# Kernel optimization log

Hardware: AMD Instinct MI355X
Metric: run time of the kernel (lower is better)

## Reference

```python
import jax, jax.numpy as jnp
import numpy as np

WINDOW_SIZE = 11

def _gauss_window(ws):
    x = np.arange(ws, dtype=np.float32)
    g = np.exp(-0.5 * (x - (ws - 1) / 2.0) ** 2 / 0.5 ** 2)
    g = g / g.sum()
    w = np.outer(g, g)
    return jnp.asarray(w[None, None], dtype=jnp.float32)  # [1,1,ws,ws]

_SOBEL_X = jnp.asarray(np.array([[-1, 0, 1], [-2, 0, 2], [-1, 0, 1]], np.float32)[None, None])
_SOBEL_Y = jnp.asarray(np.array([[1, 2, 1], [0, 0, 0], [-1, -2, -1]], np.float32)[None, None])

def _conv2d(x, k, pad):
    # x: [B,1,H,W], k: [1,1,kh,kw], 'same'-style explicit padding
    return jax.lax.conv_general_dilated(
        x, k, window_strides=(1, 1), padding=[(pad, pad), (pad, pad)],
        dimension_numbers=("NCHW", "OIHW", "NCHW"))

def _sobel(x):
    return jnp.abs(_conv2d(x, _SOBEL_X, 1)) + jnp.abs(_conv2d(x, _SOBEL_Y, 1))

def setup_inputs() -> dict:
    key = jax.random.key(0)
    kA, kB, kF, kS = jax.random.split(key, 4)
    shape = (32, 1, 512, 512)
    return {
        "image_A": jax.random.uniform(kA, shape, dtype=jnp.float32),
        "image_B": jax.random.uniform(kB, shape, dtype=jnp.float32),
        "image_fused": jax.random.uniform(kF, shape, dtype=jnp.float32),
        "fuse_scheme": jax.random.randint(kS, (32,), 0, 2, dtype=jnp.int64),
    }

def reference(image_A, image_B, image_fused, fuse_scheme):
    ws = WINDOW_SIZE
    pad = ws // 2
    window = _gauss_window(ws)
    scheme = fuse_scheme.reshape(-1, 1, 1, 1)

    # masked construction of the pseudo-reference image_AB
    avg_AB = (image_A + image_B) * 0.5
    max_AB = jnp.maximum(image_A, image_B)
    image_AB = jnp.where(scheme == 0, avg_AB,
                         jnp.where(scheme == 1, max_AB, jnp.zeros_like(image_fused)))
    l_loss = jnp.mean(jnp.abs(image_AB - image_fused))

    # SSIM-style local statistics
    mu_A = _conv2d(image_A, window, pad)
    mu_B = _conv2d(image_B, window, pad)
    mu_f = _conv2d(image_fused, window, pad)
    sigma_A_sq = _conv2d(image_A ** 2, window, pad) - mu_A ** 2
    sigma_B_sq = _conv2d(image_B ** 2, window, pad) - mu_B ** 2
    sigma_f_sq = _conv2d(image_fused ** 2, window, pad) - mu_f ** 2
    sigma_Af = _conv2d(image_A * image_fused, window, pad) - mu_A * mu_f
    sigma_Bf = _conv2d(image_B * image_fused, window, pad) - mu_B * mu_f

    C = 0.03 ** 2
    cs1 = (2 * sigma_Af + C) / (sigma_A_sq + sigma_f_sq + C)
    cs2 = (2 * sigma_Bf + C) / (sigma_B_sq + sigma_f_sq + C)
    cs_map = 0.5 * cs1 + 0.5 * cs2
    cs_loss = 1.0 - (cs_map.mean() + 1.0) / 2.0

    grad_loss = jnp.mean(jnp.abs(_sobel(image_fused) -
                                 jnp.maximum(_sobel(image_A), _sobel(image_B))))
    return l_loss + 0.0 * cs_loss + grad_loss
```

## Files before the change

kernel.cpp:

```cpp
#include <hip/hip_runtime.h>

#define BATCH 32
#define H 512
#define W 512
#define N_TOT (BATCH * H * W)
#define BAND 8
#define NBLOCKS 1024


template <bool USE_PARTIALS>
__global__ __launch_bounds__(256)
void fusion_loss_kernel(const float* __restrict__ A,
                        const float* __restrict__ B,
                        const float* __restrict__ F,
                        const int* __restrict__ scheme_arr,
                        float* __restrict__ sink)
{
    __shared__ float red[4];

    const int t    = threadIdx.x;
    const int lane = t & 63;
    const int ty   = t >> 6;
    const int wave = blockIdx.x * 4 + ty;
    const int half = wave & 1;
    const int band = wave >> 1;
    const int b    = band >> 6;
    const int r0   = (band & 63) << 3;
    const int x0   = (half << 8) + (lane << 2);
    const int base = b * (H * W);
    const int scheme = scheme_arr[b];
    const bool has_l = (x0 > 0);
    const bool has_r = (x0 + 4 < W);

    const float* __restrict__ imgs[3] = {A, B, F};

    float4 rc[3][4];
    float  rl[3][4];
    float  rh[3][4];

    auto load_row = [&](int y, int slot) {
        const bool rv = (unsigned)y < (unsigned)H;
#pragma unroll
        for (int im = 0; im < 3; ++im) {
            float4 c = make_float4(0.f, 0.f, 0.f, 0.f);
            float lf = 0.f, rt = 0.f;
            if (rv) {
                const float* row = imgs[im] + base + y * W;
                c  = *reinterpret_cast<const float4*>(row + x0);
                lf = has_l ? row[x0 - 1] : 0.f;
                rt = has_r ? row[x0 + 4] : 0.f;
            }
            rc[im][slot] = c;
            rl[im][slot] = lf;
            rh[im][slot] = rt;
        }
    };

    load_row(r0 - 1, 3);
    load_row(r0,     0);
    load_row(r0 + 1, 1);

    float acc = 0.f;

#pragma unroll
    for (int k = 0; k < BAND; ++k) {
        if (k < BAND - 1) load_row(r0 + k + 2, (k + 2) & 3);

        const int sm = (k + 3) & 3;
        const int sc = k & 3;
        const int sp = (k + 1) & 3;

        float sobM[4];
#pragma unroll
        for (int im = 0; im < 3; ++im) {
            float gx[4], gy[4];
            {
                const float4 c4 = rc[im][sm];
                const float v[6] = {rl[im][sm], c4.x, c4.y, c4.z, c4.w, rh[im][sm]};
#pragma unroll
                for (int j = 0; j < 4; ++j) {
                    gx[j] = v[j + 2] - v[j];
                    gy[j] = v[j] + 2.f * v[j + 1] + v[j + 2];
                }
            }
            {
                const float4 c4 = rc[im][sc];
                const float v[6] = {rl[im][sc], c4.x, c4.y, c4.z, c4.w, rh[im][sc]};
#pragma unroll
                for (int j = 0; j < 4; ++j)
                    gx[j] += 2.f * (v[j + 2] - v[j]);
            }
            {
                const float4 c4 = rc[im][sp];
                const float v[6] = {rl[im][sp], c4.x, c4.y, c4.z, c4.w, rh[im][sp]};
#pragma unroll
                for (int j = 0; j < 4; ++j) {
                    gx[j] += v[j + 2] - v[j];
                    gy[j] -= v[j] + 2.f * v[j + 1] + v[j + 2];
                }
            }
#pragma unroll
            for (int j = 0; j < 4; ++j) {
                const float sob = fabsf(gx[j]) + fabsf(gy[j]);
                if (im == 0)      sobM[j] = sob;
                else if (im == 1) sobM[j] = fmaxf(sobM[j], sob);
                else              acc += fabsf(sob - sobM[j]);
            }
        }

        {
            const float4 a4 = rc[0][sc], b4 = rc[1][sc], f4 = rc[2][sc];
            const float av[4] = {a4.x, a4.y, a4.z, a4.w};
            const float bv[4] = {b4.x, b4.y, b4.z, b4.w};
            const float fv[4] = {f4.x, f4.y, f4.z, f4.w};
#pragma unroll
            for (int j = 0; j < 4; ++j) {
                const float ab = (scheme == 0) ? 0.5f * (av[j] + bv[j])
                               : (scheme == 1) ? fmaxf(av[j], bv[j])
                               : 0.f;
                acc += fabsf(ab - fv[j]);
            }
        }
    }

#pragma unroll
    for (int off = 32; off > 0; off >>= 1)
        acc += __shfl_down(acc, off, 64);
    if (lane == 0) red[ty] = acc;
    __syncthreads();
    if (t == 0) {
        const float s = red[0] + red[1] + red[2] + red[3];
        if (USE_PARTIALS)
            sink[blockIdx.x] = s;
        else
            atomicAdd(sink, s * (1.0f / (float)N_TOT));
    }
}

__global__ __launch_bounds__(256)
void fusion_finish(const float* __restrict__ partials, float* __restrict__ out)
{
    __shared__ float red[4];
    const int t    = threadIdx.x;
    const int lane = t & 63;
    const int ty   = t >> 6;

    const float4 p = reinterpret_cast<const float4*>(partials)[t];
    float v = (p.x + p.y) + (p.z + p.w);
#pragma unroll
    for (int off = 32; off > 0; off >>= 1)
        v += __shfl_down(v, off, 64);
    if (lane == 0) red[ty] = v;
    __syncthreads();
    if (t == 0)
        out[0] = (red[0] + red[1] + red[2] + red[3]) * (1.0f / (float)N_TOT);
}

extern "C" void kernel_launch(void* const* d_in, const int* in_sizes, int n_in,
                              void* d_out, int out_size, void* d_ws, size_t ws_size,
                              hipStream_t stream)
{
    const float* A = (const float*)d_in[0];
    const float* B = (const float*)d_in[1];
    const float* F = (const float*)d_in[2];
    const int* scheme = (const int*)d_in[3];
    float* out = (float*)d_out;

    if (d_ws != nullptr && ws_size >= NBLOCKS * sizeof(float)) {
        float* partials = (float*)d_ws;
        fusion_loss_kernel<true><<<dim3(NBLOCKS), dim3(256), 0, stream>>>(
            A, B, F, scheme, partials);
        fusion_finish<<<dim3(1), dim3(256), 0, stream>>>(partials, out);
    } else {
        hipMemsetAsync(out, 0, sizeof(float), stream);
        fusion_loss_kernel<false><<<dim3(NBLOCKS), dim3(256), 0, stream>>>(
            A, B, F, scheme, out);
    }
}
```

Measured before the change: 128.7 us.

## Stage rows into an LDS ring via global_load_lds and double the band height

Replaces per-wave direct global loads of the three images, including scalar halo loads, with async global-to-LDS copies into a six-slot ring buffer shared by the block. Each block now covers a 16-row band, and wave pairs split even and odd rows while reading 3x3 windows from LDS. The aim is to remove the redundant unaligned halo loads and overlap staging of the next rows with compute. The cost is a block-wide barrier every step, added LDS traffic, and half as many blocks.

```diff
diff --git a/kernel.cpp b/kernel.cpp
--- a/kernel.cpp
+++ b/kernel.cpp
@@ -1,12 +1,21 @@
 #include <hip/hip_runtime.h>
+#include <stdint.h>
 
 #define BATCH 32
 #define H 512
 #define W 512
 #define N_TOT (BATCH * H * W)
-#define BAND 8
-#define NBLOCKS 1024
+#define BAND 16
+#define STEPS (BAND / 2)
+#define NBLOCKS (BATCH * (H / BAND))
+#define RING 6
+#define ROWF 512
+#define TRIPF (3 * ROWF)
+#define LDSF (RING * TRIPF)
 
+
+#define GAS(p) ((__attribute__((address_space(1))) void*)(p))
+#define LAS(p) ((__attribute__((address_space(3))) void*)(p))
 
 template <bool USE_PARTIALS>
 __global__ __launch_bounds__(256)
@@ -16,88 +25,91 @@
                         const int* __restrict__ scheme_arr,
                         float* __restrict__ sink)
 {
+    __shared__ float sh[LDSF];
     __shared__ float red[4];
 
     const int t    = threadIdx.x;
     const int lane = t & 63;
     const int ty   = t >> 6;
-    const int wave = blockIdx.x * 4 + ty;
-    const int half = wave & 1;
-    const int band = wave >> 1;
-    const int b    = band >> 6;
-    const int r0   = (band & 63) << 3;
-    const int x0   = (half << 8) + (lane << 2);
+    const int d    = ty >> 1;
+    const int h    = ty & 1;
+    const int blk  = blockIdx.x;
+    const int b    = blk >> 5;
+    const int band = blk & 31;
+    const int r0   = band << 4;
     const int base = b * (H * W);
     const int scheme = scheme_arr[b];
-    const bool has_l = (x0 > 0);
-    const bool has_r = (x0 + 4 < W);
 
-    const float* __restrict__ imgs[3] = {A, B, F};
+    const bool edgeL = (h == 0) && (lane == 0);
+    const bool edgeR = (h == 1) && (lane == 63);
 
-    float4 rc[3][4];
-    float  rl[3][4];
-    float  rh[3][4];
-
-    auto load_row = [&](int y, int slot) {
-        const bool rv = (unsigned)y < (unsigned)H;
-#pragma unroll
-        for (int im = 0; im < 3; ++im) {
-            float4 c = make_float4(0.f, 0.f, 0.f, 0.f);
-            float lf = 0.f, rt = 0.f;
-            if (rv) {
-                const float* row = imgs[im] + base + y * W;
-                c  = *reinterpret_cast<const float4*>(row + x0);
-                lf = has_l ? row[x0 - 1] : 0.f;
-                rt = has_r ? row[x0 + 4] : 0.f;
+    auto stage = [&](int s0, int ng) {
+        for (int i = 0; ; ++i) {
+            const int g = ty + (i << 2);
+            if (g >= ng) break;
+            const int trip = g / 6;
+            const int sub  = g - 6 * trip;
+            const int img  = sub >> 1;
+            const int hh   = sub & 1;
+            const int s    = s0 + trip;
+            const int slot = s % RING;
+            const int y    = r0 - 1 + s;
+            float* ldst = &sh[slot * TRIPF + img * ROWF + (hh << 8)];
+            if ((unsigned)y < (unsigned)H) {
+                const float* ip = (img == 0) ? A : (img == 1) ? B : F;
+                const float* gsrc = ip + base + y * W + (hh << 8) + (lane << 2);
+                __builtin_amdgcn_global_load_lds(GAS(gsrc), LAS(ldst), 16, 0, 0);
+            } else {
+                *reinterpret_cast<float4*>(ldst + (lane << 2)) =
+                    make_float4(0.f, 0.f, 0.f, 0.f);
             }
-            rc[im][slot] = c;
-            rl[im][slot] = lf;
-            rh[im][slot] = rt;
         }
     };
 
-    load_row(r0 - 1, 3);
-    load_row(r0,     0);
-    load_row(r0 + 1, 1);
+    auto load_win = [&](float (*w)[6], int seqz) {
+        const int slot = seqz % RING;
+        const float* srow = &sh[slot * TRIPF];
+        const int ci = lane << 2;
+#pragma unroll
+        for (int im = 0; im < 3; ++im) {
+            const float* rowp = srow + im * ROWF + (h << 8);
+            const float4 c = *reinterpret_cast<const float4*>(rowp + ci);
+            const int li = edgeL ? ci : ci - 1;
+            const int ri = edgeR ? ci + 3 : ci + 4;
+            float l = rowp[li];
+            float r = rowp[ri];
+            if (edgeL) l = 0.f;
+            if (edgeR) r = 0.f;
+            w[im][0] = l;   w[im][1] = c.x; w[im][2] = c.y;
+            w[im][3] = c.z; w[im][4] = c.w; w[im][5] = r;
+        }
+    };
+
+    stage(0, 24);
+    __syncthreads();
+
+    float wm[3][6], wc[3][6], wp[3][6];
+    load_win(wm, d);
 
     float acc = 0.f;
 
-#pragma unroll
-    for (int k = 0; k < BAND; ++k) {
-        if (k < BAND - 1) load_row(r0 + k + 2, (k + 2) & 3);
+    for (int p = 0; p < STEPS; ++p) {
+        if (p < STEPS - 1) stage(2 * p + 4, 12);
 
-        const int sm = (k + 3) & 3;
-        const int sc = k & 3;
-        const int sp = (k + 1) & 3;
+        load_win(wc, d + 2 * p + 1);
+        load_win(wp, d + 2 * p + 2);
 
         float sobM[4];
 #pragma unroll
         for (int im = 0; im < 3; ++im) {
             float gx[4], gy[4];
-            {
-                const float4 c4 = rc[im][sm];
-                const float v[6] = {rl[im][sm], c4.x, c4.y, c4.z, c4.w, rh[im][sm]};
 #pragma unroll
-                for (int j = 0; j < 4; ++j) {
-                    gx[j] = v[j + 2] - v[j];
-                    gy[j] = v[j] + 2.f * v[j + 1] + v[j + 2];
-                }
-            }
-            {
-                const float4 c4 = rc[im][sc];
-                const float v[6] = {rl[im][sc], c4.x, c4.y, c4.z, c4.w, rh[im][sc]};
-#pragma unroll
-                for (int j = 0; j < 4; ++j)
-                    gx[j] += 2.f * (v[j + 2] - v[j]);
-            }
-            {
-                const float4 c4 = rc[im][sp];
-                const float v[6] = {rl[im][sp], c4.x, c4.y, c4.z, c4.w, rh[im][sp]};
-#pragma unroll
-                for (int j = 0; j < 4; ++j) {
-                    gx[j] += v[j + 2] - v[j];
-                    gy[j] -= v[j] + 2.f * v[j + 1] + v[j + 2];
-                }
+            for (int j = 0; j < 4; ++j) {
+                gx[j] = (wm[im][j + 2] - wm[im][j])
+                      + 2.f * (wc[im][j + 2] - wc[im][j])
+                      + (wp[im][j + 2] - wp[im][j]);
+                gy[j] = (wm[im][j] + 2.f * wm[im][j + 1] + wm[im][j + 2])
+                      - (wp[im][j] + 2.f * wp[im][j + 1] + wp[im][j + 2]);
             }
 #pragma unroll
             for (int j = 0; j < 4; ++j) {
@@ -108,19 +120,24 @@
             }
         }
 
-        {
-            const float4 a4 = rc[0][sc], b4 = rc[1][sc], f4 = rc[2][sc];
-            const float av[4] = {a4.x, a4.y, a4.z, a4.w};
-            const float bv[4] = {b4.x, b4.y, b4.z, b4.w};
-            const float fv[4] = {f4.x, f4.y, f4.z, f4.w};
 #pragma unroll
-            for (int j = 0; j < 4; ++j) {
-                const float ab = (scheme == 0) ? 0.5f * (av[j] + bv[j])
-                               : (scheme == 1) ? fmaxf(av[j], bv[j])
-                               : 0.f;
-                acc += fabsf(ab - fv[j]);
-            }
+        for (int j = 0; j < 4; ++j) {
+            const float av = wc[0][j + 1];
+            const float bv = wc[1][j + 1];
+            const float fv = wc[2][j + 1];
+            const float ab = (scheme == 0) ? 0.5f * (av + bv)
+                           : (scheme == 1) ? fmaxf(av, bv)
+                           : 0.f;
+            acc += fabsf(ab - fv);
         }
+
+#pragma unroll
+        for (int im = 0; im < 3; ++im)
+#pragma unroll
+            for (int k = 0; k < 6; ++k)
+                wm[im][k] = wp[im][k];
+
+        __syncthreads();
     }
 
 #pragma unroll
```

After: 176.6 us. 37.2% more time.

## Process one row per wave with full-row lanes and shuffle-based halos

Applied to the files above, without the earlier changes.

Replaces the 8-row rolling band per wave with one output row per wave, where each lane covers 8 contiguous pixels of the full 512-wide row. Horizontal halo values come from cross-lane shuffles instead of extra scalar global loads, and blocks are remapped with an XCD-style interleave. This gives many more blocks (4096) with less per-thread state and a higher occupancy hint. In exchange, each input row is now loaded three times (above, center, below), which raises global/L2 traffic compared with the band reuse. The finish kernel is widened to reduce 4096 partials.

```diff
diff --git a/kernel.cpp b/kernel.cpp
--- a/kernel.cpp
+++ b/kernel.cpp
@@ -4,12 +4,13 @@
 #define H 512
 #define W 512
 #define N_TOT (BATCH * H * W)
-#define BAND 8
-#define NBLOCKS 1024
+#define ROWS_TOTAL (BATCH * H)
+#define NBLOCKS (ROWS_TOTAL / 4)
+#define WS_FLOATS NBLOCKS
 
 
 template <bool USE_PARTIALS>
-__global__ __launch_bounds__(256)
+__global__ __launch_bounds__(256, 4)
 void fusion_loss_kernel(const float* __restrict__ A,
                         const float* __restrict__ B,
                         const float* __restrict__ F,
@@ -21,117 +22,104 @@
     const int t    = threadIdx.x;
     const int lane = t & 63;
     const int ty   = t >> 6;
-    const int wave = blockIdx.x * 4 + ty;
-    const int half = wave & 1;
-    const int band = wave >> 1;
-    const int b    = band >> 6;
-    const int r0   = (band & 63) << 3;
-    const int x0   = (half << 8) + (lane << 2);
-    const int base = b * (H * W);
+
+    const int bid = blockIdx.x;
+    const int lb  = (bid & 7) * (NBLOCKS / 8) + (bid >> 3);
+
+    const int gy  = (lb << 2) | ty;
+    const int b   = gy >> 9;
+    const int y   = gy & (H - 1);
+    const int x0  = lane << 3;
     const int scheme = scheme_arr[b];
-    const bool has_l = (x0 > 0);
-    const bool has_r = (x0 + 4 < W);
 
-    const float* __restrict__ imgs[3] = {A, B, F};
+    const int off = gy * W + x0;
+    const bool vm = (y > 0);
+    const bool vp = (y < H - 1);
 
-    float4 rc[3][4];
-    float  rl[3][4];
-    float  rh[3][4];
-
-    auto load_row = [&](int y, int slot) {
-        const bool rv = (unsigned)y < (unsigned)H;
+    float4 u0[3][3], u1[3][3];
+    {
+        const float* ptr[3] = {A + off, B + off, F + off};
 #pragma unroll
         for (int im = 0; im < 3; ++im) {
-            float4 c = make_float4(0.f, 0.f, 0.f, 0.f);
-            float lf = 0.f, rt = 0.f;
-            if (rv) {
-                const float* row = imgs[im] + base + y * W;
-                c  = *reinterpret_cast<const float4*>(row + x0);
-                lf = has_l ? row[x0 - 1] : 0.f;
-                rt = has_r ? row[x0 + 4] : 0.f;
+            const float* p = ptr[im];
+            u0[im][1] = *reinterpret_cast<const float4*>(p);
+            u1[im][1] = *reinterpret_cast<const float4*>(p + 4);
+            if (vm) {
+                u0[im][0] = *reinterpret_cast<const float4*>(p - W);
+                u1[im][0] = *reinterpret_cast<const float4*>(p - W + 4);
+            } else {
+                u0[im][0] = make_float4(0.f, 0.f, 0.f, 0.f);
+                u1[im][0] = make_float4(0.f, 0.f, 0.f, 0.f);
             }
-            rc[im][slot] = c;
-            rl[im][slot] = lf;
-            rh[im][slot] = rt;
+            if (vp) {
+                u0[im][2] = *reinterpret_cast<const float4*>(p + W);
+                u1[im][2] = *reinterpret_cast<const float4*>(p + W + 4);
+            } else {
+                u0[im][2] = make_float4(0.f, 0.f, 0.f, 0.f);
+                u1[im][2] = make_float4(0.f, 0.f, 0.f, 0.f);
+            }
         }
-    };
-
-    load_row(r0 - 1, 3);
-    load_row(r0,     0);
-    load_row(r0 + 1, 1);
+    }
 
     float acc = 0.f;
 
 #pragma unroll
-    for (int k = 0; k < BAND; ++k) {
-        if (k < BAND - 1) load_row(r0 + k + 2, (k + 2) & 3);
+    for (int hh = 0; hh < 2; ++hh) {
+        const float4 a4 = hh ? u1[0][1] : u0[0][1];
+        const float4 b4 = hh ? u1[1][1] : u0[1][1];
+        const float4 f4 = hh ? u1[2][1] : u0[2][1];
+        const float av[4] = {a4.x, a4.y, a4.z, a4.w};
+        const float bv[4] = {b4.x, b4.y, b4.z, b4.w};
+        const float fv[4] = {f4.x, f4.y, f4.z, f4.w};
+#pragma unroll
+        for (int j = 0; j < 4; ++j) {
+            const float ab = (scheme == 0) ? 0.5f * (av[j] + bv[j])
+                           : (scheme == 1) ? fmaxf(av[j], bv[j])
+                           : 0.f;
+            acc += fabsf(ab - fv[j]);
+        }
+    }
 
-        const int sm = (k + 3) & 3;
-        const int sc = k & 3;
-        const int sp = (k + 1) & 3;
-
-        float sobM[4];
+    float sobM[8];
 #pragma unroll
-        for (int im = 0; im < 3; ++im) {
-            float gx[4], gy[4];
-            {
-                const float4 c4 = rc[im][sm];
-                const float v[6] = {rl[im][sm], c4.x, c4.y, c4.z, c4.w, rh[im][sm]};
+    for (int im = 0; im < 3; ++im) {
+        float v[3][10];
 #pragma unroll
-                for (int j = 0; j < 4; ++j) {
-                    gx[j] = v[j + 2] - v[j];
-                    gy[j] = v[j] + 2.f * v[j + 1] + v[j + 2];
-                }
-            }
-            {
-                const float4 c4 = rc[im][sc];
-                const float v[6] = {rl[im][sc], c4.x, c4.y, c4.z, c4.w, rh[im][sc]};
+        for (int r = 0; r < 3; ++r) {
+            const float4 a = u0[im][r];
+            const float4 c = u1[im][r];
+            float lN = __shfl_up(c.w, 1, 64);
+            float rN = __shfl_down(a.x, 1, 64);
+            if (lane == 0)  lN = 0.f;
+            if (lane == 63) rN = 0.f;
+            v[r][0] = lN;
+            v[r][1] = a.x; v[r][2] = a.y; v[r][3] = a.z; v[r][4] = a.w;
+            v[r][5] = c.x; v[r][6] = c.y; v[r][7] = c.z; v[r][8] = c.w;
+            v[r][9] = rN;
+        }
 #pragma unroll
-                for (int j = 0; j < 4; ++j)
-                    gx[j] += 2.f * (v[j + 2] - v[j]);
-            }
-            {
-                const float4 c4 = rc[im][sp];
-                const float v[6] = {rl[im][sp], c4.x, c4.y, c4.z, c4.w, rh[im][sp]};
-#pragma unroll
-                for (int j = 0; j < 4; ++j) {
-                    gx[j] += v[j + 2] - v[j];
-                    gy[j] -= v[j] + 2.f * v[j + 1] + v[j + 2];
-                }
-            }
-#pragma unroll
-            for (int j = 0; j < 4; ++j) {
-                const float sob = fabsf(gx[j]) + fabsf(gy[j]);
-                if (im == 0)      sobM[j] = sob;
-                else if (im == 1) sobM[j] = fmaxf(sobM[j], sob);
-                else              acc += fabsf(sob - sobM[j]);
-            }
-        }
-
-        {
-            const float4 a4 = rc[0][sc], b4 = rc[1][sc], f4 = rc[2][sc];
-            const float av[4] = {a4.x, a4.y, a4.z, a4.w};
-            const float bv[4] = {b4.x, b4.y, b4.z, b4.w};
-            const float fv[4] = {f4.x, f4.y, f4.z, f4.w};
-#pragma unroll
-            for (int j = 0; j < 4; ++j) {
-                const float ab = (scheme == 0) ? 0.5f * (av[j] + bv[j])
-                               : (scheme == 1) ? fmaxf(av[j], bv[j])
-                               : 0.f;
-                acc += fabsf(ab - fv[j]);
-            }
+        for (int j = 0; j < 8; ++j) {
+            const float gx = (v[0][j + 2] - v[0][j])
+                           + 2.f * (v[1][j + 2] - v[1][j])
+                           + (v[2][j + 2] - v[2][j]);
+            const float gyv = (v[0][j] + 2.f * v[0][j + 1] + v[0][j + 2])
+                            - (v[2][j] + 2.f * v[2][j + 1] + v[2][j + 2]);
+            const float sob = fabsf(gx) + fabsf(gyv);
+            if (im == 0)      sobM[j] = sob;
+            else if (im == 1) sobM[j] = fmaxf(sobM[j], sob);
+            else              acc += fabsf(sob - sobM[j]);
         }
     }
 
 #pragma unroll
-    for (int off = 32; off > 0; off >>= 1)
-        acc += __shfl_down(acc, off, 64);
+    for (int offp = 32; offp > 0; offp >>= 1)
+        acc += __shfl_down(acc, offp, 64);
     if (lane == 0) red[ty] = acc;
     __syncthreads();
     if (t == 0) {
         const float s = red[0] + red[1] + red[2] + red[3];
         if (USE_PARTIALS)
-            sink[blockIdx.x] = s;
+            sink[bid] = s;
         else
             atomicAdd(sink, s * (1.0f / (float)N_TOT));
     }
@@ -145,12 +133,16 @@
     const int lane = t & 63;
     const int ty   = t >> 6;
 
-    const float4 p = reinterpret_cast<const float4*>(partials)[t];
-    float v = (p.x + p.y) + (p.z + p.w);
+    float s = 0.f;
+#pragma unroll
+    for (int k = 0; k < 4; ++k) {
+        const float4 p = reinterpret_cast<const float4*>(partials)[t + 256 * k];
+        s += (p.x + p.y) + (p.z + p.w);
+    }
 #pragma unroll
     for (int off = 32; off > 0; off >>= 1)
-        v += __shfl_down(v, off, 64);
-    if (lane == 0) red[ty] = v;
+        s += __shfl_down(s, off, 64);
+    if (lane == 0) red[ty] = s;
     __syncthreads();
     if (t == 0)
         out[0] = (red[0] + red[1] + red[2] + red[3]) * (1.0f / (float)N_TOT);
@@ -166,7 +158,7 @@
     const int* scheme = (const int*)d_in[3];
     float* out = (float*)d_out;
 
-    if (d_ws != nullptr && ws_size >= NBLOCKS * sizeof(float)) {
+    if (d_ws != nullptr && ws_size >= WS_FLOATS * sizeof(float)) {
         float* partials = (float*)d_ws;
         fusion_loss_kernel<true><<<dim3(NBLOCKS), dim3(256), 0, stream>>>(
             A, B, F, scheme, partials);
```

Result: faster. 121.4 us, median of 2 (-5.6%).
